# Performance work log

Hardware: AMD Instinct MI355X
Metric: run time of the kernel (lower is better)

## Reference

```python
import jax, jax.numpy as jnp
import numpy as np

# shift search range (matches init_kwargs)
MIN_SX, MAX_SX = -4, 4
MIN_SY, MAX_SY = -4, 4
B, C, H, W = 4, 3, 512, 512


def _shift(x, sx, sy):
    """torch.roll on dims (1,2) of a [C,H,W] tensor, zeroing wrapped rows/cols.

    Equivalent to AutomatedShiftFix.shift: positive sx zeros rows [:sx],
    negative sx zeros rows [sx:]; same for sy on the W axis.
    """
    h, w = x.shape[1], x.shape[2]
    shifted = jnp.roll(x, (sx, sy), axis=(1, 2))
    i = jnp.arange(h)[:, None]   # [H,1]
    j = jnp.arange(w)[None, :]   # [1,W]
    mask_h = jnp.where(sx >= 0, i >= sx, i < h + sx)
    mask_w = jnp.where(sy >= 0, j >= sy, j < w + sy)
    mask = (mask_h & mask_w).astype(x.dtype)  # [H,W]
    return shifted * mask[None]


def _all_shifts():
    sx = jnp.arange(MIN_SX, MAX_SX + 1)
    sy = jnp.arange(MIN_SY, MAX_SY + 1)
    # outer loop over shift_x, inner over shift_y -> 'ij' matches torch ordering
    return jnp.stack(jnp.meshgrid(sx, sy, indexing="ij"), axis=-1).reshape(-1, 2)  # [Ns,2]


def setup_inputs() -> dict:
    key = jax.random.key(0)
    k1, k2 = jax.random.split(key)
    x_ref = jax.random.normal(k1, (B, C, H, W), dtype=jnp.float32)
    x = jax.random.normal(k2, (B, C, H, W), dtype=jnp.float32)
    return {"x_ref": x_ref, "x": x}


def reference(x_ref, x):
    shifts = _all_shifts()  # [Ns,2] int32

    def sims_one(xr, xi):  # xr, xi: [C,H,W]
        # similarity for every candidate shift: sum over (C,H,W) of shifted*ref
        return jax.vmap(lambda s: jnp.sum(_shift(xi, s[0], s[1]) * xr))(shifts)  # [Ns]

    sims = jax.vmap(sims_one)(x_ref, x)          # [B, Ns]
    best = jnp.argmax(sims, axis=1)              # [B]
    best_shifts = shifts[best]                   # [B, 2]
    out = jax.vmap(lambda xi, s: _shift(xi, s[0], s[1]))(x, best_shifts)  # [B,C,H,W]
    return out, best_shifts
```

## Files before the change

### kernel.cpp

```cpp
#include <hip/hip_runtime.h>

#define BB 4
#define CC 3
#define HH 512
#define WW 512
#define NS 81
#define IMG (HH * WW)
#define CHW (CC * IMG)
#define STRIP 32
#define NSTRIP (HH / STRIP)
#define NBLK (BB * CC * NSTRIP * 9)

#define BEST_OFF (NBLK * 9 * sizeof(float))

__global__ __launch_bounds__(256, 8) void k_sims(const float* __restrict__ xref,
                                                 const float* __restrict__ x,
                                                 float* __restrict__ partials) {
    int bid  = blockIdx.x;
    int sxi  = bid % 9;
    int tmp  = bid / 9;
    int strip = tmp % NSTRIP;
    int bc   = tmp / NSTRIP;
    const float* xp = x    + (size_t)bc * IMG;
    const float* rp = xref + (size_t)bc * IMG;
    int tid  = threadIdx.x;
    int lane = tid & 63;
    int wave = tid >> 6;
    int j0   = lane << 3;
    int sx   = sxi - 4;

    float acc[9];
#pragma unroll
    for (int s = 0; s < 9; ++s) acc[s] = 0.f;

#pragma unroll
    for (int rr = 0; rr < 8; ++rr) {
        int ip = strip * STRIP + wave * 8 + rr;
        int ii = ip + sx;
        if ((unsigned)ii >= HH) continue;

        const float* xrow = xp + ip * WW + j0;
        float x8[8];
        *(float4*)(x8)     = *(const float4*)(xrow);
        *(float4*)(x8 + 4) = *(const float4*)(xrow + 4);

        const float* rrow = rp + ii * WW + j0;
        float w[16];
        if (j0 >= 4) *(float4*)(w) = *(const float4*)(rrow - 4);
        else { w[0] = w[1] = w[2] = w[3] = 0.f; }
        *(float4*)(w + 4) = *(const float4*)(rrow);
        *(float4*)(w + 8) = *(const float4*)(rrow + 4);
        if (j0 + 12 <= WW) *(float4*)(w + 12) = *(const float4*)(rrow + 8);
        else { w[12] = w[13] = w[14] = w[15] = 0.f; }

#pragma unroll
        for (int syi = 0; syi < 9; ++syi)
#pragma unroll
            for (int k = 0; k < 8; ++k)
                acc[syi] += x8[k] * w[k + syi];
    }

    __shared__ float part[4][9];
#pragma unroll
    for (int s = 0; s < 9; ++s) {
        float v = acc[s];
        for (int off = 32; off; off >>= 1) v += __shfl_down(v, off, 64);
        if (lane == 0) part[wave][s] = v;
    }
    __syncthreads();
    if (tid < 9)
        partials[bid * 9 + tid] = part[0][tid] + part[1][tid]
                                + part[2][tid] + part[3][tid];
}

__global__ __launch_bounds__(512) void k_argmax(const float* __restrict__ partials,
                                                int* __restrict__ best,
                                                float* __restrict__ outTail) {
    int b = blockIdx.x;
    int t = threadIdx.x;
    __shared__ double lds[486];
    __shared__ double vals[NS];
    if (t < 486) {
        int slot = t / 6;
        int sub  = t % 6;
        int sxi = slot / 9, syi = slot % 9;
        double acc = 0.0;
#pragma unroll
        for (int k = 0; k < 8; ++k) {
            int q  = sub * 8 + k;
            int c  = q >> 4;
            int st = q & 15;
            int pb = ((b * CC + c) * NSTRIP + st) * 9 + sxi;
            acc += (double)partials[pb * 9 + syi];
        }
        lds[t] = acc;
    }
    __syncthreads();
    if (t < NS) {
        double s = 0.0;
#pragma unroll
        for (int k = 0; k < 6; ++k) s += lds[t * 6 + k];
        vals[t] = s;
    }
    __syncthreads();
    if (t == 0) {
        double bv = vals[0];
        int bi = 0;
        for (int s = 1; s < NS; ++s)
            if (vals[s] > bv) { bv = vals[s]; bi = s; }
        int sx = bi / 9 - 4;
        int sy = bi % 9 - 4;
        best[b * 2]     = sx;
        best[b * 2 + 1] = sy;
        outTail[b * 2]     = (float)sx;
        outTail[b * 2 + 1] = (float)sy;
    }
}

__global__ __launch_bounds__(256) void k_apply(const float* __restrict__ x,
                                               const int* __restrict__ best,
                                               float* __restrict__ out) {
    int blk = blockIdx.x;
    int bc  = blk >> 8;
    int tid = threadIdx.x;
    int row = ((blk & 255) << 1) + (tid >> 7);
    int j0  = (tid & 127) << 2;
    int b   = bc / CC;
    int sx  = best[b * 2];
    int sy  = best[b * 2 + 1];
    int is  = row - sx;
    float4 v = make_float4(0.f, 0.f, 0.f, 0.f);
    if ((unsigned)is < HH) {
        const float* src = x + (size_t)bc * IMG + is * WW;
        int js0 = j0 - sy;
        if (js0 >= 0 && js0 + 3 < WW) {
            v = *(const float4*)(src + js0);
        } else {
            float* vv = (float*)&v;
#pragma unroll
            for (int k = 0; k < 4; ++k) {
                int js = js0 + k;
                if ((unsigned)js < WW) vv[k] = src[js];
            }
        }
    }
    *(float4*)(out + (size_t)bc * IMG + row * WW + j0) = v;
}

extern "C" void kernel_launch(void* const* d_in, const int* in_sizes, int n_in,
                              void* d_out, int out_size, void* d_ws, size_t ws_size,
                              hipStream_t stream) {
    const float* xref = (const float*)d_in[0];
    const float* x    = (const float*)d_in[1];
    float* out = (float*)d_out;

    float* partials = (float*)d_ws;
    int*   best     = (int*)((char*)d_ws + BEST_OFF);

    k_sims<<<NBLK, 256, 0, stream>>>(xref, x, partials);

    k_argmax<<<BB, 512, 0, stream>>>(partials, best, out + (size_t)BB * CHW);

    int applyBlocks = (BB * CC * HH) / 2;
    k_apply<<<applyBlocks, 256, 0, stream>>>(x, best, out);
}
```

Measured before the change: 110.2 us.

## Stage reference strips in LDS and cover all row shifts per block

The similarity kernel changes from one row-shift per block to one block per 8-row strip that handles all 9 row-shifts, one wave per shift. The reference rows plus a 4-row halo are staged once into shared memory, split into even and odd float4 banks so each lane's shifted window comes from LDS instead of repeated global loads. This removes the 9x redundant global or L2 reads of the reference image and drops the cross-wave reduction barrier, since each wave writes its own 9 partials. The cost is more, smaller per-block partials for the argmax kernel to reduce, a larger block size under tighter register bounds, and the x rows still being loaded by every wave.

```diff
diff --git a/kernel.cpp b/kernel.cpp
--- a/kernel.cpp
+++ b/kernel.cpp
@@ -7,51 +7,64 @@
 #define NS 81
 #define IMG (HH * WW)
 #define CHW (CC * IMG)
-#define STRIP 32
+#define STRIP 8
 #define NSTRIP (HH / STRIP)
-#define NBLK (BB * CC * NSTRIP * 9)
+#define NBLK (BB * CC * NSTRIP)
 
-#define BEST_OFF (NBLK * 9 * sizeof(float))
+#define BEST_OFF (NBLK * NS * sizeof(float))
 
-__global__ __launch_bounds__(256, 8) void k_sims(const float* __restrict__ xref,
+__global__ __launch_bounds__(576, 6) void k_sims(const float* __restrict__ xref,
                                                  const float* __restrict__ x,
                                                  float* __restrict__ partials) {
-    int bid  = blockIdx.x;
-    int sxi  = bid % 9;
-    int tmp  = bid / 9;
-    int strip = tmp % NSTRIP;
-    int bc   = tmp / NSTRIP;
+    int bid   = blockIdx.x;
+    int strip = bid & (NSTRIP - 1);
+    int bc    = bid >> 6;
+    int r0    = strip * STRIP;
     const float* xp = x    + (size_t)bc * IMG;
     const float* rp = xref + (size_t)bc * IMG;
     int tid  = threadIdx.x;
     int lane = tid & 63;
-    int wave = tid >> 6;
+    int wav  = tid >> 6;
     int j0   = lane << 3;
-    int sx   = sxi - 4;
+
+    __shared__ float4 refE[16][65];
+    __shared__ float4 refO[16][65];
+
+    for (int idx = tid; idx < 16 * 128; idx += 576) {
+        int r  = idx >> 7;
+        int gc = idx & 127;
+        int g  = r0 - 4 + r;
+        float4 v = make_float4(0.f, 0.f, 0.f, 0.f);
+        if ((unsigned)g < HH) v = *(const float4*)(rp + g * WW + gc * 4);
+        int k = gc + 1;
+        if (k & 1) refO[r][k >> 1] = v;
+        else       refE[r][k >> 1] = v;
+    }
+    if (tid < 32) {
+        float4 z = make_float4(0.f, 0.f, 0.f, 0.f);
+        if (tid < 16) refE[tid][0] = z;
+        else          refO[tid - 16][64] = z;
+    }
+    __syncthreads();
 
     float acc[9];
 #pragma unroll
     for (int s = 0; s < 9; ++s) acc[s] = 0.f;
 
 #pragma unroll
-    for (int rr = 0; rr < 8; ++rr) {
-        int ip = strip * STRIP + wave * 8 + rr;
-        int ii = ip + sx;
-        if ((unsigned)ii >= HH) continue;
-
+    for (int rr = 0; rr < STRIP; ++rr) {
+        int ip = r0 + rr;
         const float* xrow = xp + ip * WW + j0;
         float x8[8];
         *(float4*)(x8)     = *(const float4*)(xrow);
         *(float4*)(x8 + 4) = *(const float4*)(xrow + 4);
 
-        const float* rrow = rp + ii * WW + j0;
+        int lr = rr + wav;
         float w[16];
-        if (j0 >= 4) *(float4*)(w) = *(const float4*)(rrow - 4);
-        else { w[0] = w[1] = w[2] = w[3] = 0.f; }
-        *(float4*)(w + 4) = *(const float4*)(rrow);
-        *(float4*)(w + 8) = *(const float4*)(rrow + 4);
-        if (j0 + 12 <= WW) *(float4*)(w + 12) = *(const float4*)(rrow + 8);
-        else { w[12] = w[13] = w[14] = w[15] = 0.f; }
+        *(float4*)(w)      = refE[lr][lane];
+        *(float4*)(w + 4)  = refO[lr][lane];
+        *(float4*)(w + 8)  = refE[lr][lane + 1];
+        *(float4*)(w + 12) = refO[lr][lane + 1];
 
 #pragma unroll
         for (int syi = 0; syi < 9; ++syi)
@@ -60,17 +73,12 @@
                 acc[syi] += x8[k] * w[k + syi];
     }
 
-    __shared__ float part[4][9];
 #pragma unroll
     for (int s = 0; s < 9; ++s) {
         float v = acc[s];
         for (int off = 32; off; off >>= 1) v += __shfl_down(v, off, 64);
-        if (lane == 0) part[wave][s] = v;
+        if (lane == 0) partials[bid * NS + wav * 9 + s] = v;
     }
-    __syncthreads();
-    if (tid < 9)
-        partials[bid * 9 + tid] = part[0][tid] + part[1][tid]
-                                + part[2][tid] + part[3][tid];
 }
 
 __global__ __launch_bounds__(512) void k_argmax(const float* __restrict__ partials,
@@ -83,15 +91,14 @@
     if (t < 486) {
         int slot = t / 6;
         int sub  = t % 6;
-        int sxi = slot / 9, syi = slot % 9;
         double acc = 0.0;
-#pragma unroll
-        for (int k = 0; k < 8; ++k) {
-            int q  = sub * 8 + k;
-            int c  = q >> 4;
-            int st = q & 15;
-            int pb = ((b * CC + c) * NSTRIP + st) * 9 + sxi;
-            acc += (double)partials[pb * 9 + syi];
+#pragma unroll 8
+        for (int k = 0; k < 32; ++k) {
+            int q  = sub * 32 + k;
+            int c  = q >> 6;
+            int st = q & 63;
+            int pb = (b * CC + c) * NSTRIP + st;
+            acc += (double)partials[pb * NS + slot];
         }
         lds[t] = acc;
     }
@@ -157,7 +164,7 @@
     float* partials = (float*)d_ws;
     int*   best     = (int*)((char*)d_ws + BEST_OFF);
 
-    k_sims<<<NBLK, 256, 0, stream>>>(xref, x, partials);
+    k_sims<<<NBLK, 576, 0, stream>>>(xref, x, partials);
 
     k_argmax<<<BB, 512, 0, stream>>>(partials, best, out + (size_t)BB * CHW);
 
```

Measured after the change: 331.1 us. 3.01x slower.
